# Performance work log

Hardware: AMD Instinct MI355X
Metric: run time of the kernel (lower is better)

Reference implementation:

```python
import jax, jax.numpy as jnp
import numpy as np

N = 512
NODE_IN = 64
NODE_OUT = 64
ED_IN = 32
ED_OUT = 32
STATE = 80  # must satisfy 2*NODE_IN + ED_IN == 2*STATE
SLOPE = 0.1
EPS = 1e-5


def setup_inputs() -> dict:
    key = jax.random.key(0)
    ks = jax.random.split(key, 10)
    def lin(k, out_f, in_f):
        return jax.random.normal(k, (out_f, in_f), jnp.float32) / np.sqrt(in_f).astype(np.float32)
    x = jax.random.normal(ks[0], (N, NODE_IN), jnp.float32)
    edge_attr = jax.random.normal(ks[1], (N * N, ED_IN), jnp.float32)
    mask = jax.random.randint(ks[2], (N * N, 1), 0, 2).astype(jnp.int32)
    return {
        "x": x,
        "edge_attr": edge_attr,
        "mask": mask,
        "W_nu": lin(ks[3], NODE_OUT, NODE_IN),
        "b_nu": jnp.zeros((NODE_OUT,), jnp.float32),
        "W_h2": lin(ks[4], STATE, 2 * STATE),
        "b_h2": jnp.zeros((STATE,), jnp.float32),
        "W_eo": lin(ks[5], ED_OUT, STATE),
        "b_eo": jnp.zeros((ED_OUT,), jnp.float32),
        "e_vec": jax.random.normal(ks[6], (2 * NODE_OUT + ED_OUT,), jnp.float32) * 0.1,
        "bn_n_w": jnp.ones((NODE_OUT,), jnp.float32),
        "bn_n_b": jnp.zeros((NODE_OUT,), jnp.float32),
        "bn_e_w": jnp.ones((ED_OUT,), jnp.float32),
        "bn_e_b": jnp.zeros((ED_OUT,), jnp.float32),
    }


def _lrelu(v):
    return jax.nn.leaky_relu(v, SLOPE)


def _bn(v, w, b):
    # BatchNorm1d, training-mode (batch stats, biased variance)
    mu = v.mean(axis=0)
    var = v.var(axis=0)
    return (v - mu) / jnp.sqrt(var + EPS) * w + b


def reference(x, edge_attr, mask, W_nu, b_nu, W_h2, b_h2, W_eo, b_eo, e_vec,
              bn_n_w, bn_n_b, bn_e_w, bn_e_b):
    n = x.shape[0]
    m = mask.astype(x.dtype)  # [N*N, 1]
    # triplet_e[i*N+j] = [x_i, edge_attr_{ij}, x_j]
    src = jnp.repeat(x, n, axis=0)          # [N*N, NODE_IN]
    dst = jnp.tile(x, (n, 1))               # [N*N, NODE_IN]
    triplet_e = jnp.concatenate([src, edge_attr, dst], axis=-1)  # [N*N, 2*STATE]
    # NOTE: ed_trans_layer / ed_hidden_1 outputs are dead code in the source.
    h = _lrelu(triplet_e @ W_h2.T + b_h2)                 # [N*N, STATE]
    new_edge_attr = _lrelu(h @ W_eo.T + b_eo)             # [N*N, ED_OUT]
    new_edge_attr = new_edge_attr * m
    xn = _lrelu(x @ W_nu.T + b_nu)                        # [N, NODE_OUT]
    triplet_n = jnp.concatenate(
        [jnp.repeat(xn, n, axis=0), new_edge_attr, jnp.tile(xn, (n, 1))], axis=-1
    ).reshape(n, n, 2 * NODE_OUT + ED_OUT)
    scores = _lrelu(jnp.einsum("ijd,d->ij", triplet_n, e_vec))  # [N, N]
    att = jax.nn.softmax(scores, axis=1)
    att = (att.reshape(n * n, 1) * m).reshape(n, n)
    # dropout disabled (deterministic / eval)
    new_x = att @ xn                                       # [N, NODE_OUT]
    new_x = _bn(new_x, bn_n_w, bn_n_b)
    new_edge_attr = _bn(new_edge_attr, bn_e_w, bn_e_b)
    return new_x, new_edge_attr
```

## Files before the change

kernel.cpp:

```cpp
#include <hip/hip_runtime.h>

#define SLOPE 0.1f
#define EPS 1e-5f

typedef __bf16 bf16x8 __attribute__((ext_vector_type(8)));
typedef unsigned short u16x8 __attribute__((ext_vector_type(8)));
typedef float f32x4 __attribute__((ext_vector_type(4)));
typedef unsigned u32x4 __attribute__((ext_vector_type(4)));

#define WS_ESC 0
#define WS_ESH 32
#define WS_A 64
#define WS_B 576
#define WS_XN 1088
#define WS_NEWX 33856
#define WS_P1B 66624
#define WS_P2 107584
#define WS_PART 148544
#define WSH_WB 362624
#define WSH_WO 367744
#define WSH_NE 370816

__device__ __forceinline__ float lrelu(float v) { return v > 0.f ? v : SLOPE * v; }
__device__ __forceinline__ unsigned short f2bf(float f) {
  unsigned x = __float_as_uint(f);
  return (unsigned short)((x + 0x7fffu + ((x >> 16) & 1u)) >> 16);
}
__device__ __forceinline__ float bf2f(unsigned short u) {
  return __uint_as_float(((unsigned)u) << 16);
}

__global__ void __launch_bounds__(256) k1(const float* __restrict__ x,
                                          const float* __restrict__ W_nu,
                                          const float* __restrict__ b_nu,
                                          const float* __restrict__ W_h2,
                                          const float* __restrict__ b_h2,
                                          const float* __restrict__ W_eo,
                                          const float* __restrict__ ev,
                                          float* ws) {
  int blk = blockIdx.x;
  int tid = threadIdx.x;
  unsigned short* wsh = (unsigned short*)ws;
  if (blk < 128) {
    __shared__ float wlds[64 * 65];
#pragma unroll
    for (int it = 0; it < 16; it++) {
      int idx = it * 256 + tid;
      wlds[(idx >> 6) * 65 + (idx & 63)] = W_nu[idx];
    }
    int gid = blk * 256 + tid;
    if (gid < 5120) {
      wsh[WSH_WB + gid] = f2bf(W_h2[(gid >> 6) * 160 + 64 + (gid & 63)]);
    } else if (gid < 8192) {
      int idx = gid - 5120;
      int n = idx / 96, kk = idx - 96 * n;
      wsh[WSH_WO + idx] = (kk < 80) ? f2bf(W_eo[n * 80 + kk]) : (unsigned short)0;
    }
    __syncthreads();
    int i = blk * 4 + (tid >> 6);
    int c = tid & 63;
    float acc = b_nu[c];
    const float* xr = x + i * 64;
#pragma unroll 8
    for (int k = 0; k < 64; k++) acc += xr[k] * wlds[c * 65 + k];
    float xnv = lrelu(acc);
    ws[WS_XN + i * 64 + c] = xnv;
    float va = xnv * ev[c];
    float vb = xnv * ev[96 + c];
#pragma unroll
    for (int off = 32; off >= 1; off >>= 1) {
      va += __shfl_xor(va, off, 64);
      vb += __shfl_xor(vb, off, 64);
    }
    if (c == 0) { ws[WS_A + i] = va; ws[WS_B + i] = vb; }
  } else {
    int b2 = blk - 128;
    int bm = b2 & 7, bn = b2 >> 3;
    int wave = tid >> 6, lane = tid & 63;
    int c16 = lane & 15, q = lane >> 4;
    int n = bn * 16 + c16;
    const float* wrow = (n < 80) ? (W_h2 + n * 160) : (W_h2 + (n - 80) * 160 + 96);
    int mrow = bm * 64 + wave * 16 + c16;
    bf16x8 bfr[2], afr[2];
#pragma unroll
    for (int ks = 0; ks < 2; ks++) {
      const float* bs = wrow + ks * 32 + q * 8;
      const float* as = x + mrow * 64 + ks * 32 + q * 8;
      u16x8 ub, ua;
#pragma unroll
      for (int jj = 0; jj < 8; jj++) { ub[jj] = f2bf(bs[jj]); ua[jj] = f2bf(as[jj]); }
      bfr[ks] = __builtin_bit_cast(bf16x8, ub);
      afr[ks] = __builtin_bit_cast(bf16x8, ua);
    }
    float bias = (n < 80) ? b_h2[n] : 0.f;
    f32x4 acc = {bias, bias, bias, bias};
    acc = __builtin_amdgcn_mfma_f32_16x16x32_bf16(afr[0], bfr[0], acc, 0, 0, 0);
    acc = __builtin_amdgcn_mfma_f32_16x16x32_bf16(afr[1], bfr[1], acc, 0, 0, 0);
#pragma unroll
    for (int r = 0; r < 4; r++) {
      int mm = bm * 64 + wave * 16 + q * 4 + r;
      if (n < 80) ws[WS_P1B + mm * 80 + n] = acc[r];
      else        ws[WS_P2 + mm * 80 + (n - 80)] = acc[r];
    }
  }
}

__global__ void __launch_bounds__(512) k2(const float* __restrict__ ea,
                                          const int* __restrict__ mask,
                                          const float* __restrict__ b_eo,
                                          const float* __restrict__ ev,
                                          float* ws) {
  __shared__ unsigned short ht[128 * 104];
  __shared__ float srow[512];
  __shared__ float mlds[512];
  __shared__ float p1s[80];
  __shared__ float wred[2][8][32];
  __shared__ float nx[8][64];
  __shared__ float red[8];
  int tid = threadIdx.x;
  int w = tid >> 6, lane = tid & 63;
  int c16 = lane & 15, q = lane >> 4;
  int i = blockIdx.x;
  const unsigned short* wsh = (const unsigned short*)ws;
  unsigned* ne32 = (unsigned*)((unsigned short*)ws + WSH_NE);

  mlds[tid] = mask[i * 512 + tid] ? 1.f : 0.f;
  if (tid < 80) p1s[tid] = ws[WS_P1B + i * 80 + tid];

  bf16x8 wb[5];
#pragma unroll
  for (int t = 0; t < 5; t++)
    wb[t] = __builtin_bit_cast(
        bf16x8, *(const u16x8*)(wsh + WSH_WB + (t * 16 + c16) * 64 + q * 8));
  bf16x8 wo[2][3];
#pragma unroll
  for (int t2 = 0; t2 < 2; t2++)
#pragma unroll
    for (int s = 0; s < 3; s++)
      wo[t2][s] = __builtin_bit_cast(
          bf16x8,
          *(const u16x8*)(wsh + WSH_WO + (t2 * 16 + c16) * 96 + s * 32 + q * 8));
  float beo0 = b_eo[c16], beo1 = b_eo[16 + c16];
  float eve0 = ev[64 + c16], eve1 = ev[80 + c16];
  float a_i = ws[WS_A + i];
  __syncthreads();

  float scs0 = 0.f, scss0 = 0.f, scs1 = 0.f, scss1 = 0.f;
#pragma unroll 1
  for (int mt = 0; mt < 4; mt++) {
    int jb = w * 64 + mt * 16;
    bf16x8 af;
    {
      const float* src = ea + (i * 512 + jb + c16) * 32 + q * 8;
      u16x8 u;
#pragma unroll
      for (int jj = 0; jj < 8; jj++) u[jj] = f2bf(src[jj]);
      af = __builtin_bit_cast(bf16x8, u);
    }
    f32x4 acc[5];
#pragma unroll
    for (int t = 0; t < 5; t++) {
      int n = t * 16 + c16;
      float p1v = p1s[n];
#pragma unroll
      for (int r = 0; r < 4; r++)
        acc[t][r] = p1v + ws[WS_P2 + (jb + q * 4 + r) * 80 + n];
    }
#pragma unroll
    for (int t = 0; t < 5; t++)
      acc[t] = __builtin_amdgcn_mfma_f32_16x16x32_bf16(af, wb[t], acc[t], 0, 0, 0);
#pragma unroll
    for (int t = 0; t < 5; t++)
#pragma unroll
      for (int r = 0; r < 4; r++)
        ht[(w * 16 + q * 4 + r) * 104 + t * 16 + c16] = f2bf(lrelu(acc[t][r]));
    f32x4 acc2[2] = {{0.f, 0.f, 0.f, 0.f}, {0.f, 0.f, 0.f, 0.f}};
    int hrow = w * 16 + c16;
#pragma unroll
    for (int s = 0; s < 3; s++) {
      int kk = s * 32 + q * 8;
      u16x8 hb = {0, 0, 0, 0, 0, 0, 0, 0};
      if (kk < 80) hb = *(const u16x8*)&ht[hrow * 104 + kk];
      bf16x8 ha = __builtin_bit_cast(bf16x8, hb);
      acc2[0] = __builtin_amdgcn_mfma_f32_16x16x32_bf16(ha, wo[0][s], acc2[0], 0, 0, 0);
      acc2[1] = __builtin_amdgcn_mfma_f32_16x16x32_bf16(ha, wo[1][s], acc2[1], 0, 0, 0);
    }
    float se[4];
#pragma unroll
    for (int r = 0; r < 4; r++) {
      int jl = jb + q * 4 + r;
      float mf = mlds[jl];
      float v0 = lrelu(acc2[0][r] + beo0) * mf;
      float v1 = lrelu(acc2[1][r] + beo1) * mf;
      scs0 += v0; scss0 += v0 * v0;
      scs1 += v1; scss1 += v1 * v1;
      ne32[(i * 512 + jl) * 16 + c16] =
          (unsigned)f2bf(v0) | ((unsigned)f2bf(v1) << 16);
      float s = v0 * eve0 + v1 * eve1;
#pragma unroll
      for (int off = 8; off >= 1; off >>= 1) s += __shfl_xor(s, off, 64);
      se[r] = s;
    }
    if (c16 < 4) {
      int jl = jb + q * 4 + c16;
      float s = (c16 == 0) ? se[0] : (c16 == 1) ? se[1] : (c16 == 2) ? se[2] : se[3];
      srow[jl] = lrelu(a_i + ws[WS_B + jl] + s);
    }
  }
  scs0 += __shfl_xor(scs0, 16, 64); scs0 += __shfl_xor(scs0, 32, 64);
  scss0 += __shfl_xor(scss0, 16, 64); scss0 += __shfl_xor(scss0, 32, 64);
  scs1 += __shfl_xor(scs1, 16, 64); scs1 += __shfl_xor(scs1, 32, 64);
  scss1 += __shfl_xor(scss1, 16, 64); scss1 += __shfl_xor(scss1, 32, 64);
  if (q == 0) {
    wred[0][w][c16] = scs0; wred[0][w][16 + c16] = scs1;
    wred[1][w][c16] = scss0; wred[1][w][16 + c16] = scss1;
  }
  __syncthreads();
  if (tid < 64) {
    int half = tid >> 5, col = tid & 31;
    float v = 0.f;
#pragma unroll
    for (int ww = 0; ww < 8; ww++) v += wred[half][ww][col];
    ws[WS_PART + i * 64 + tid] = v;
  }
  float p = __expf(srow[tid]);
  float sm = p;
#pragma unroll
  for (int off = 32; off >= 1; off >>= 1) sm += __shfl_xor(sm, off, 64);
  if (lane == 0) red[w] = sm;
  __syncthreads();
  float tot = red[0] + red[1] + red[2] + red[3] + red[4] + red[5] + red[6] + red[7];
  srow[tid] = p * (1.f / tot) * mlds[tid];
  float accv = 0.f;
#pragma unroll 4
  for (int u = 0; u < 64; u++) {
    int j = w * 64 + u;
    accv += srow[j] * ws[WS_XN + j * 64 + lane];
  }
  nx[w][lane] = accv;
  __syncthreads();
  if (tid < 64) {
    float s = 0.f;
#pragma unroll
    for (int ww = 0; ww < 8; ww++) s += nx[ww][tid];
    ws[WS_NEWX + i * 64 + tid] = s;
  }
}

__global__ void __launch_bounds__(512) k3(const float* __restrict__ bn_e_w,
                                          const float* __restrict__ bn_e_b,
                                          float* ws) {
  __shared__ float nx[8][64];
  int tid = threadIdx.x;
  int g = tid >> 6, c = tid & 63;
  float a = 0.f;
  for (int s = g; s < 512; s += 8) a += ws[WS_PART + s * 64 + c];
  nx[g][c] = a;
  __syncthreads();
  if (tid < 64) {
    float t = 0.f;
#pragma unroll
    for (int g2 = 0; g2 < 8; g2++) t += nx[g2][tid];
    nx[0][tid] = t;
  }
  __syncthreads();
  if (tid < 32) {
    float mean = nx[0][tid] * (1.f / 262144.f);
    float var = nx[0][tid + 32] * (1.f / 262144.f) - mean * mean;
    float s = bn_e_w[tid] * rsqrtf(fmaxf(var, 0.f) + EPS);
    ws[WS_ESC + tid] = s;
    ws[WS_ESH + tid] = bn_e_b[tid] - mean * s;
  }
}

__global__ void __launch_bounds__(256) k5(const float* __restrict__ bn_n_w,
                                          const float* __restrict__ bn_n_b,
                                          const float* __restrict__ ws,
                                          float* __restrict__ out) {
  int blk = blockIdx.x, tid = threadIdx.x;
  if (blk < 8) {
    __shared__ float s1[4][64], s2[4][64], scl[64], sh[64];
    int c = tid & 63, g = tid >> 6;
    float a = 0.f, b = 0.f;
#pragma unroll 4
    for (int u = 0; u < 128; u++) {
      float v = ws[WS_NEWX + (g * 128 + u) * 64 + c];
      a += v;
      b += v * v;
    }
    s1[g][c] = a;
    s2[g][c] = b;
    __syncthreads();
    if (tid < 64) {
      float sum = s1[0][tid] + s1[1][tid] + s1[2][tid] + s1[3][tid];
      float ssq = s2[0][tid] + s2[1][tid] + s2[2][tid] + s2[3][tid];
      float mean = sum * (1.f / 512.f);
      float var = ssq * (1.f / 512.f) - mean * mean;
      float s = bn_n_w[tid] * rsqrtf(fmaxf(var, 0.f) + EPS);
      scl[tid] = s;
      sh[tid] = bn_n_b[tid] - mean * s;
    }
    __syncthreads();
#pragma unroll 4
    for (int u = 0; u < 16; u++) {
      int idx = blk * 4096 + u * 256 + tid;
      int c2 = idx & 63;
      out[idx] = ws[WS_NEWX + idx] * scl[c2] + sh[c2];
    }
  } else {
    const unsigned* ne32 = (const unsigned*)((const unsigned short*)ws + WSH_NE);
    int b4 = ((blk - 8) * 256 + tid) * 4;
    u32x4 raw = *(const u32x4*)(ne32 + b4);
    int e32 = (b4 >> 4) * 32;
    int cb = b4 & 15;
    f32x4 esc0 = *(const f32x4*)(ws + WS_ESC + cb);
    f32x4 esc1 = *(const f32x4*)(ws + WS_ESC + 16 + cb);
    f32x4 esh0 = *(const f32x4*)(ws + WS_ESH + cb);
    f32x4 esh1 = *(const f32x4*)(ws + WS_ESH + 16 + cb);
    f32x4 lo, hi;
#pragma unroll
    for (int u = 0; u < 4; u++) {
      lo[u] = bf2f((unsigned short)(raw[u] & 0xffffu)) * esc0[u] + esh0[u];
      hi[u] = bf2f((unsigned short)(raw[u] >> 16)) * esc1[u] + esh1[u];
    }
    float* oe = out + 32768;
    *(f32x4*)(oe + e32 + cb) = lo;
    *(f32x4*)(oe + e32 + 16 + cb) = hi;
  }
}

extern "C" void kernel_launch(void* const* d_in, const int* in_sizes, int n_in,
                              void* d_out, int out_size, void* d_ws, size_t ws_size,
                              hipStream_t stream) {
  const float* x = (const float*)d_in[0];
  const float* ea = (const float*)d_in[1];
  const int* mask = (const int*)d_in[2];
  const float* Wnu = (const float*)d_in[3];
  const float* bnu = (const float*)d_in[4];
  const float* Wh2 = (const float*)d_in[5];
  const float* bh2 = (const float*)d_in[6];
  const float* Weo = (const float*)d_in[7];
  const float* beo = (const float*)d_in[8];
  const float* ev = (const float*)d_in[9];
  const float* bnw = (const float*)d_in[10];
  const float* bnb = (const float*)d_in[11];
  const float* bew = (const float*)d_in[12];
  const float* beb = (const float*)d_in[13];
  float* ws = (float*)d_ws;
  float* out = (float*)d_out;

  k1<<<208, 256, 0, stream>>>(x, Wnu, bnu, Wh2, bh2, Weo, ev, ws);
  k2<<<512, 512, 0, stream>>>(ea, mask, beo, ev, ws);
  k3<<<1, 512, 0, stream>>>(bew, beb, ws);
  k5<<<4104, 256, 0, stream>>>(bnw, bnb, ws, out);
}
```

Baseline: 170.7 us.

## Compute dst projection in k2 via MFMA and fold BN-stats kernel into k2

Drops the precomputed P2 (x_j projection) table: k2 now does three MFMA passes over the edge features and bf16 copies of x_j, with the W_h2 slices prepacked in bf16 by k1. The separate single-block k3 that reduced edge BN statistics is folded into k2 through a last-block atomic counter and threadfence. W_eo fragments are loaded per iteration instead of being held in registers, and launch bounds request 4 blocks per CU. The aim is to cut the global P2 reads and one kernel launch, in exchange for extra MFMA work and the serial tail run by the last block.

```diff
diff --git a/kernel.cpp b/kernel.cpp
--- a/kernel.cpp
+++ b/kernel.cpp
@@ -10,16 +10,18 @@
 
 #define WS_ESC 0
 #define WS_ESH 32
-#define WS_A 64
-#define WS_B 576
-#define WS_XN 1088
-#define WS_NEWX 33856
-#define WS_P1B 66624
-#define WS_P2 107584
-#define WS_PART 148544
-#define WSH_WB 362624
-#define WSH_WO 367744
-#define WSH_NE 370816
+#define WS_CNT 64
+#define WS_A 96
+#define WS_B 608
+#define WS_XN 1120
+#define WS_NEWX 33888
+#define WS_P1B 66656
+#define WS_PART 107616
+#define WSH_WB 280768
+#define WSH_WB2 285888
+#define WSH_WO 288448
+#define WSH_XB 291520
+#define WSH_NE 324288
 
 __device__ __forceinline__ float lrelu(float v) { return v > 0.f ? v : SLOPE * v; }
 __device__ __forceinline__ unsigned short f2bf(float f) {
@@ -49,13 +51,18 @@
       wlds[(idx >> 6) * 65 + (idx & 63)] = W_nu[idx];
     }
     int gid = blk * 256 + tid;
+    wsh[WSH_XB + gid] = f2bf(x[gid]);
     if (gid < 5120) {
       wsh[WSH_WB + gid] = f2bf(W_h2[(gid >> 6) * 160 + 64 + (gid & 63)]);
-    } else if (gid < 8192) {
+    } else if (gid < 7680) {
       int idx = gid - 5120;
+      wsh[WSH_WB2 + idx] = f2bf(W_h2[(idx >> 5) * 160 + 128 + (idx & 31)]);
+    } else if (gid < 10752) {
+      int idx = gid - 7680;
       int n = idx / 96, kk = idx - 96 * n;
       wsh[WSH_WO + idx] = (kk < 80) ? f2bf(W_eo[n * 80 + kk]) : (unsigned short)0;
     }
+    if (gid == 0) *(int*)(ws + WS_CNT) = 0;
     __syncthreads();
     int i = blk * 4 + (tid >> 6);
     int c = tid & 63;
@@ -79,7 +86,7 @@
     int wave = tid >> 6, lane = tid & 63;
     int c16 = lane & 15, q = lane >> 4;
     int n = bn * 16 + c16;
-    const float* wrow = (n < 80) ? (W_h2 + n * 160) : (W_h2 + (n - 80) * 160 + 96);
+    const float* wrow = W_h2 + n * 160;
     int mrow = bm * 64 + wave * 16 + c16;
     bf16x8 bfr[2], afr[2];
 #pragma unroll
@@ -92,24 +99,25 @@
       bfr[ks] = __builtin_bit_cast(bf16x8, ub);
       afr[ks] = __builtin_bit_cast(bf16x8, ua);
     }
-    float bias = (n < 80) ? b_h2[n] : 0.f;
+    float bias = b_h2[n];
     f32x4 acc = {bias, bias, bias, bias};
     acc = __builtin_amdgcn_mfma_f32_16x16x32_bf16(afr[0], bfr[0], acc, 0, 0, 0);
     acc = __builtin_amdgcn_mfma_f32_16x16x32_bf16(afr[1], bfr[1], acc, 0, 0, 0);
 #pragma unroll
     for (int r = 0; r < 4; r++) {
       int mm = bm * 64 + wave * 16 + q * 4 + r;
-      if (n < 80) ws[WS_P1B + mm * 80 + n] = acc[r];
-      else        ws[WS_P2 + mm * 80 + (n - 80)] = acc[r];
-    }
-  }
-}
-
-__global__ void __launch_bounds__(512) k2(const float* __restrict__ ea,
-                                          const int* __restrict__ mask,
-                                          const float* __restrict__ b_eo,
-                                          const float* __restrict__ ev,
-                                          float* ws) {
+      ws[WS_P1B + mm * 80 + n] = acc[r];
+    }
+  }
+}
+
+__global__ void __launch_bounds__(512, 4) k2(const float* __restrict__ ea,
+                                             const int* __restrict__ mask,
+                                             const float* __restrict__ b_eo,
+                                             const float* __restrict__ ev,
+                                             const float* __restrict__ bn_e_w,
+                                             const float* __restrict__ bn_e_b,
+                                             float* ws) {
   __shared__ unsigned short ht[128 * 104];
   __shared__ float srow[512];
   __shared__ float mlds[512];
@@ -117,6 +125,7 @@
   __shared__ float wred[2][8][32];
   __shared__ float nx[8][64];
   __shared__ float red[8];
+  __shared__ int lastf;
   int tid = threadIdx.x;
   int w = tid >> 6, lane = tid & 63;
   int c16 = lane & 15, q = lane >> 4;
@@ -127,19 +136,15 @@
   mlds[tid] = mask[i * 512 + tid] ? 1.f : 0.f;
   if (tid < 80) p1s[tid] = ws[WS_P1B + i * 80 + tid];
 
-  bf16x8 wb[5];
-#pragma unroll
-  for (int t = 0; t < 5; t++)
-    wb[t] = __builtin_bit_cast(
-        bf16x8, *(const u16x8*)(wsh + WSH_WB + (t * 16 + c16) * 64 + q * 8));
-  bf16x8 wo[2][3];
-#pragma unroll
-  for (int t2 = 0; t2 < 2; t2++)
-#pragma unroll
-    for (int s = 0; s < 3; s++)
-      wo[t2][s] = __builtin_bit_cast(
-          bf16x8,
-          *(const u16x8*)(wsh + WSH_WO + (t2 * 16 + c16) * 96 + s * 32 + q * 8));
+  bf16x8 wb0[5], wb1[5], wb2f[5];
+#pragma unroll
+  for (int t = 0; t < 5; t++) {
+    int n = t * 16 + c16;
+    wb0[t] = __builtin_bit_cast(bf16x8, *(const u16x8*)(wsh + WSH_WB + n * 64 + q * 8));
+    wb1[t] = __builtin_bit_cast(bf16x8,
+                                *(const u16x8*)(wsh + WSH_WB + n * 64 + 32 + q * 8));
+    wb2f[t] = __builtin_bit_cast(bf16x8, *(const u16x8*)(wsh + WSH_WB2 + n * 32 + q * 8));
+  }
   float beo0 = b_eo[c16], beo1 = b_eo[16 + c16];
   float eve0 = ev[64 + c16], eve1 = ev[80 + c16];
   float a_i = ws[WS_A + i];
@@ -149,26 +154,33 @@
 #pragma unroll 1
   for (int mt = 0; mt < 4; mt++) {
     int jb = w * 64 + mt * 16;
-    bf16x8 af;
+    bf16x8 af0;
     {
       const float* src = ea + (i * 512 + jb + c16) * 32 + q * 8;
       u16x8 u;
 #pragma unroll
       for (int jj = 0; jj < 8; jj++) u[jj] = f2bf(src[jj]);
-      af = __builtin_bit_cast(bf16x8, u);
-    }
+      af0 = __builtin_bit_cast(bf16x8, u);
+    }
+    bf16x8 af1 = __builtin_bit_cast(
+        bf16x8, *(const u16x8*)(wsh + WSH_XB + (jb + c16) * 64 + q * 8));
+    bf16x8 af2 = __builtin_bit_cast(
+        bf16x8, *(const u16x8*)(wsh + WSH_XB + (jb + c16) * 64 + 32 + q * 8));
     f32x4 acc[5];
 #pragma unroll
     for (int t = 0; t < 5; t++) {
-      int n = t * 16 + c16;
-      float p1v = p1s[n];
-#pragma unroll
-      for (int r = 0; r < 4; r++)
-        acc[t][r] = p1v + ws[WS_P2 + (jb + q * 4 + r) * 80 + n];
+      float p1v = p1s[t * 16 + c16];
+      acc[t] = {p1v, p1v, p1v, p1v};
     }
 #pragma unroll
     for (int t = 0; t < 5; t++)
-      acc[t] = __builtin_amdgcn_mfma_f32_16x16x32_bf16(af, wb[t], acc[t], 0, 0, 0);
+      acc[t] = __builtin_amdgcn_mfma_f32_16x16x32_bf16(af0, wb0[t], acc[t], 0, 0, 0);
+#pragma unroll
+    for (int t = 0; t < 5; t++)
+      acc[t] = __builtin_amdgcn_mfma_f32_16x16x32_bf16(af1, wb1[t], acc[t], 0, 0, 0);
+#pragma unroll
+    for (int t = 0; t < 5; t++)
+      acc[t] = __builtin_amdgcn_mfma_f32_16x16x32_bf16(af2, wb2f[t], acc[t], 0, 0, 0);
 #pragma unroll
     for (int t = 0; t < 5; t++)
 #pragma unroll
@@ -182,8 +194,12 @@
       u16x8 hb = {0, 0, 0, 0, 0, 0, 0, 0};
       if (kk < 80) hb = *(const u16x8*)&ht[hrow * 104 + kk];
       bf16x8 ha = __builtin_bit_cast(bf16x8, hb);
-      acc2[0] = __builtin_amdgcn_mfma_f32_16x16x32_bf16(ha, wo[0][s], acc2[0], 0, 0, 0);
-      acc2[1] = __builtin_amdgcn_mfma_f32_16x16x32_bf16(ha, wo[1][s], acc2[1], 0, 0, 0);
+      bf16x8 wo0 = __builtin_bit_cast(
+          bf16x8, *(const u16x8*)(wsh + WSH_WO + c16 * 96 + s * 32 + q * 8));
+      bf16x8 wo1 = __builtin_bit_cast(
+          bf16x8, *(const u16x8*)(wsh + WSH_WO + (16 + c16) * 96 + s * 32 + q * 8));
+      acc2[0] = __builtin_amdgcn_mfma_f32_16x16x32_bf16(ha, wo0, acc2[0], 0, 0, 0);
+      acc2[1] = __builtin_amdgcn_mfma_f32_16x16x32_bf16(ha, wo1, acc2[1], 0, 0, 0);
     }
     float se[4];
 #pragma unroll
@@ -194,8 +210,7 @@
       float v1 = lrelu(acc2[1][r] + beo1) * mf;
       scs0 += v0; scss0 += v0 * v0;
       scs1 += v1; scss1 += v1 * v1;
-      ne32[(i * 512 + jl) * 16 + c16] =
-          (unsigned)f2bf(v0) | ((unsigned)f2bf(v1) << 16);
+      ne32[(i * 512 + jl) * 16 + c16] = (unsigned)f2bf(v0) | ((unsigned)f2bf(v1) << 16);
       float s = v0 * eve0 + v1 * eve1;
 #pragma unroll
       for (int off = 8; off >= 1; off >>= 1) s += __shfl_xor(s, off, 64);
@@ -245,31 +260,32 @@
     for (int ww = 0; ww < 8; ww++) s += nx[ww][tid];
     ws[WS_NEWX + i * 64 + tid] = s;
   }
-}
-
-__global__ void __launch_bounds__(512) k3(const float* __restrict__ bn_e_w,
-                                          const float* __restrict__ bn_e_b,
-                                          float* ws) {
-  __shared__ float nx[8][64];
-  int tid = threadIdx.x;
-  int g = tid >> 6, c = tid & 63;
-  float a = 0.f;
-  for (int s = g; s < 512; s += 8) a += ws[WS_PART + s * 64 + c];
-  nx[g][c] = a;
-  __syncthreads();
-  if (tid < 64) {
-    float t = 0.f;
-#pragma unroll
-    for (int g2 = 0; g2 < 8; g2++) t += nx[g2][tid];
-    nx[0][tid] = t;
-  }
-  __syncthreads();
-  if (tid < 32) {
-    float mean = nx[0][tid] * (1.f / 262144.f);
-    float var = nx[0][tid + 32] * (1.f / 262144.f) - mean * mean;
-    float s = bn_e_w[tid] * rsqrtf(fmaxf(var, 0.f) + EPS);
-    ws[WS_ESC + tid] = s;
-    ws[WS_ESH + tid] = bn_e_b[tid] - mean * s;
+  if (tid == 0) {
+    __threadfence();
+    lastf = (atomicAdd((int*)(ws + WS_CNT), 1) == 511);
+  }
+  __syncthreads();
+  if (lastf) {
+    __threadfence();
+    int g = tid >> 6, c = tid & 63;
+    float a = 0.f;
+    for (int s = g; s < 512; s += 8) a += ws[WS_PART + s * 64 + c];
+    nx[g][c] = a;
+    __syncthreads();
+    if (tid < 64) {
+      float t = 0.f;
+#pragma unroll
+      for (int g2 = 0; g2 < 8; g2++) t += nx[g2][tid];
+      srow[tid] = t;
+    }
+    __syncthreads();
+    if (tid < 32) {
+      float mean = srow[tid] * (1.f / 262144.f);
+      float var = srow[tid + 32] * (1.f / 262144.f) - mean * mean;
+      float s = bn_e_w[tid] * rsqrtf(fmaxf(var, 0.f) + EPS);
+      ws[WS_ESC + tid] = s;
+      ws[WS_ESH + tid] = bn_e_b[tid] - mean * s;
+    }
   }
 }
 
@@ -349,8 +365,7 @@
   float* ws = (float*)d_ws;
   float* out = (float*)d_out;
 
-  k1<<<208, 256, 0, stream>>>(x, Wnu, bnu, Wh2, bh2, Weo, ev, ws);
-  k2<<<512, 512, 0, stream>>>(ea, mask, beo, ev, ws);
-  k3<<<1, 512, 0, stream>>>(bew, beb, ws);
+  k1<<<168, 256, 0, stream>>>(x, Wnu, bnu, Wh2, bh2, Weo, ev, ws);
+  k2<<<512, 512, 0, stream>>>(ea, mask, beo, ev, bew, beb, ws);
   k5<<<4104, 256, 0, stream>>>(bnw, bnb, ws, out);
 }
```

New measurement: 191.6 us. 12.2% more time.
